# Kernel tuning notes

Measured on AMD Instinct MI355X. Metric: run time of the kernel, lower is better.

The kernel has to match this reference:

```python
import jax, jax.numpy as jnp
import numpy as np

GROUPS = 32
HEADS = 8
EPS = 1e-5


def setup_inputs() -> dict:
    key = jax.random.key(0)
    ks = jax.random.split(key, 3)
    b, c, h, w = 8, 512, 32, 32
    x = jax.random.normal(ks[0], (b, c, h, w), dtype=jnp.float32)
    gn_w = jnp.ones((c,), jnp.float32)
    gn_b = jnp.zeros((c,), jnp.float32)
    qkv_w = jax.random.normal(ks[1], (3 * c, c), dtype=jnp.float32) * (1.0 / np.sqrt(c))
    qkv_b = jnp.zeros((3 * c,), jnp.float32)
    proj_w = jax.random.normal(ks[2], (c, c), dtype=jnp.float32) * (1.0 / np.sqrt(c))
    proj_b = jnp.zeros((c,), jnp.float32)
    return {"x": x, "gn_w": gn_w, "gn_b": gn_b, "qkv_w": qkv_w,
            "qkv_b": qkv_b, "proj_w": proj_w, "proj_b": proj_b}


def group_norm(x, weight, bias):
    b, c, h, w = x.shape
    xg = x.reshape(b, GROUPS, c // GROUPS, h, w)
    mean = xg.mean(axis=(2, 3, 4), keepdims=True)
    var = xg.var(axis=(2, 3, 4), keepdims=True)
    xn = ((xg - mean) * jax.lax.rsqrt(var + EPS)).reshape(b, c, h, w)
    return xn * weight[None, :, None, None] + bias[None, :, None, None]


def reference(x, gn_w, gn_b, qkv_w, qkv_b, proj_w, proj_b):
    b, c, h, w = x.shape
    dh = c // HEADS
    xn = group_norm(x, gn_w, gn_b)
    # 1x1 conv == per-pixel linear: (b,c,h,w) x (3c,c) -> (b,3c,h,w)
    qkv = jnp.einsum('bchw,oc->bohw', xn, qkv_w) + qkv_b[None, :, None, None]
    qkv = qkv.reshape(b, 3, HEADS, dh, h * w)  # 'three' outermost, then heads, head_dim
    q, k, v = qkv[:, 0], qkv[:, 1], qkv[:, 2]  # (b, heads, dh, hw)
    scale = dh ** (-0.5)
    attn = jax.nn.softmax(jnp.einsum('bhci,bhcj->bhij', q, k) * scale, axis=-1)
    out = jnp.einsum('bhij,bhcj->bhci', attn, v)  # (b, heads, dh, hw)
    out = out.reshape(b, c, h, w)
    out = jnp.einsum('bchw,oc->bohw', out, proj_w) + proj_b[None, :, None, None]
    return x + out
```

## Files before the change

### kernel.cpp

```cpp
#include <hip/hip_runtime.h>
#include <cstdint>
#include <cstddef>

#define BATCH 8
#define CCH   512
#define SSP   1024
#define NH    8
#define DH    64
#define O3    1536

typedef __bf16 bf16x8 __attribute__((ext_vector_type(8)));
typedef float  f32x4  __attribute__((ext_vector_type(4)));

__device__ __forceinline__ unsigned short f2bf(float f) {
    unsigned u = __builtin_bit_cast(unsigned, f);
    unsigned r = u + 0x7fffu + ((u >> 16) & 1u);
    return (unsigned short)(r >> 16);
}

__device__ __forceinline__ unsigned pk2bf(float lo, float hi) {
    unsigned ul = __builtin_bit_cast(unsigned, lo) + 0x8000u;
    unsigned uh = __builtin_bit_cast(unsigned, hi) + 0x8000u;
    return __builtin_amdgcn_perm(uh, ul, 0x07060302u);
}

__device__ __forceinline__ bf16x8 ld8(const unsigned short* p) {
    uint4 u = *(const uint4*)p;
    return __builtin_bit_cast(bf16x8, u);
}

__device__ __forceinline__ void glls16(const void* g, void* l) {
    __builtin_amdgcn_global_load_lds(
        (const __attribute__((address_space(1))) unsigned*)g,
        (__attribute__((address_space(3))) unsigned*)l, 16, 0, 0);
}

__global__ __launch_bounds__(256) void wconv2(const float* __restrict__ s1,
                                              unsigned short* __restrict__ d1, int n1,
                                              const float* __restrict__ s2,
                                              unsigned short* __restrict__ d2) {
    int i = blockIdx.x * 256 + threadIdx.x;
    const float4* sp;
    ushort4* dp;
    if (i < n1) { sp = (const float4*)s1 + i; dp = (ushort4*)d1 + i; }
    else        { sp = (const float4*)s2 + (i - n1); dp = (ushort4*)d2 + (i - n1); }
    float4 v = *sp;
    ushort4 o;
    o.x = f2bf(v.x); o.y = f2bf(v.y); o.z = f2bf(v.z); o.w = f2bf(v.w);
    *dp = o;
}

__global__ __launch_bounds__(256) void groupnorm_t(const float* __restrict__ x,
                                                   const float* __restrict__ gw,
                                                   const float* __restrict__ gb,
                                                   unsigned short* __restrict__ xnt) {
    int blk = blockIdx.x;
    int b = blk >> 5, g = blk & 31;
    const float4* xp = (const float4*)(x + (size_t)(b * CCH + g * 16) * SSP);
    int t = threadIdx.x;

    float4 vals[16];
    float sum = 0.f, ss = 0.f;
#pragma unroll
    for (int i = 0; i < 16; i++) {
        float4 v = xp[i * 256 + t];
        vals[i] = v;
        sum += (v.x + v.y) + (v.z + v.w);
        ss  += (v.x * v.x + v.y * v.y) + (v.z * v.z + v.w * v.w);
    }
#pragma unroll
    for (int o = 32; o; o >>= 1) {
        sum += __shfl_xor(sum, o, 64);
        ss  += __shfl_xor(ss,  o, 64);
    }
    __shared__ float red[8];
    if ((t & 63) == 0) { red[(t >> 6) * 2] = sum; red[(t >> 6) * 2 + 1] = ss; }
    __syncthreads();
    sum = red[0] + red[2] + red[4] + red[6];
    ss  = red[1] + red[3] + red[5] + red[7];

    float mean = sum * (1.f / 16384.f);
    float var  = ss * (1.f / 16384.f) - mean * mean;
    float rstd = rsqrtf(var + 1e-5f);

    __shared__ unsigned short tile[16][1032];
#pragma unroll
    for (int i = 0; i < 16; i++) {
        int f4 = i * 256 + t;
        int c = f4 >> 8;
        int s = (f4 & 255) * 4;
        float wsc = gw[g * 16 + c] * rstd;
        float bia = gb[g * 16 + c] - mean * wsc;
        float4 v = vals[i];
        tile[c][s + 0] = f2bf(v.x * wsc + bia);
        tile[c][s + 1] = f2bf(v.y * wsc + bia);
        tile[c][s + 2] = f2bf(v.z * wsc + bia);
        tile[c][s + 3] = f2bf(v.w * wsc + bia);
    }
    __syncthreads();

    int c2 = (t & 7) * 2, sr = t >> 3;
    unsigned short* outbase = xnt + (size_t)b * SSP * CCH + g * 16 + c2;
#pragma unroll
    for (int i = 0; i < 32; i++) {
        int s = i * 32 + sr;
        unsigned v = (unsigned)tile[c2][s] | ((unsigned)tile[c2 + 1][s] << 16);
        *(unsigned*)(outbase + (size_t)s * CCH) = v;
    }
}

__global__ __launch_bounds__(256) void gemm_qkv(const unsigned short* __restrict__ Aall,
                                                const unsigned short* __restrict__ Bw,
                                                const float* __restrict__ bias,
                                                unsigned short* __restrict__ Call,
                                                unsigned short* __restrict__ vtout) {
    const int K = 512;
    int bz = blockIdx.z;
    const unsigned short* A = Aall + (size_t)bz * SSP * CCH;
    int m0 = blockIdx.x * 128, n0 = blockIdx.y * 128;

    __shared__ unsigned short As[128 * 64], Bs[128 * 64];
    int t = threadIdx.x, wave = t >> 6, lane = t & 63;
    int quad = lane >> 4, l16 = lane & 15;
    int wm = (wave & 1) * 64, wn = (wave >> 1) * 64;

    int lrow = lane >> 3;
    int lc   = ((lane & 7) - lrow) & 7;
    const unsigned short* Ag = A  + (size_t)(m0 + wave * 32 + lrow) * K + lc * 8;
    const unsigned short* Bg = Bw + (size_t)(n0 + wave * 32 + lrow) * K + lc * 8;
    unsigned short* Asw = As + wave * 2048;
    unsigned short* Bsw = Bs + wave * 2048;

    f32x4 acc[4][4];
#pragma unroll
    for (int i = 0; i < 4; i++)
#pragma unroll
        for (int j = 0; j < 4; j++) acc[i][j] = f32x4{0.f, 0.f, 0.f, 0.f};

    int rowA = (wm + l16) * 64, rowB = (wn + l16) * 64;
    int cph[2];
#pragma unroll
    for (int kc = 0; kc < 2; kc++) cph[kc] = ((quad + 4 * kc + l16) & 7) * 8;

    for (int k0 = 0; k0 < K; k0 += 64) {
        __syncthreads();
#pragma unroll
        for (int i = 0; i < 4; i++) {
            glls16(Ag + (size_t)i * 8 * K + k0, Asw + i * 512);
            glls16(Bg + (size_t)i * 8 * K + k0, Bsw + i * 512);
        }
        __syncthreads();
#pragma unroll
        for (int kc = 0; kc < 2; kc++) {
            bf16x8 af[4], bfr[4];
#pragma unroll
            for (int i = 0; i < 4; i++) {
                af[i]  = ld8(As + rowA + i * 1024 + cph[kc]);
                bfr[i] = ld8(Bs + rowB + i * 1024 + cph[kc]);
            }
#pragma unroll
            for (int i = 0; i < 4; i++)
#pragma unroll
                for (int j = 0; j < 4; j++)
                    acc[i][j] = __builtin_amdgcn_mfma_f32_16x16x32_bf16(af[i], bfr[j], acc[i][j], 0, 0, 0);
        }
    }

    if (n0 < 1024) {
        unsigned short* Cp = Call + (size_t)bz * SSP * O3;
#pragma unroll
        for (int i = 0; i < 4; i++)
#pragma unroll
            for (int j = 0; j < 4; j++) {
                int col = n0 + wn + j * 16 + l16;
                float bv = bias[col];
#pragma unroll
                for (int r = 0; r < 4; r++) {
                    int row = m0 + wm + i * 16 + quad * 4 + r;
                    Cp[(size_t)row * O3 + col] = f2bf(acc[i][j][r] + bv);
                }
            }
    } else {
#pragma unroll
        for (int j = 0; j < 4; j++) {
            int col = n0 + wn + j * 16 + l16;
            float bv = bias[col];
            unsigned short* vp = vtout + ((size_t)bz * 512 + (col - 1024)) * SSP;
#pragma unroll
            for (int i = 0; i < 4; i++) {
                int s = m0 + wm + i * 16 + quad * 4;
                uint2 d;
                d.x = pk2bf(acc[i][j][0] + bv, acc[i][j][1] + bv);
                d.y = pk2bf(acc[i][j][2] + bv, acc[i][j][3] + bv);
                *(uint2*)(vp + s) = d;
            }
        }
    }
}

__global__ __launch_bounds__(256) void gemm_proj(const unsigned short* __restrict__ Pw,
                                                 const unsigned short* __restrict__ Oall,
                                                 const float* __restrict__ bias,
                                                 const float* __restrict__ xres,
                                                 float* __restrict__ Out) {
    const int K = 512;
    int bz = blockIdx.z;
    const unsigned short* Bv = Oall + (size_t)bz * SSP * CCH;
    int m0 = blockIdx.x * 128, n0 = blockIdx.y * 128;

    __shared__ unsigned short As[128 * 64], Bs[128 * 64];
    int t = threadIdx.x, wave = t >> 6, lane = t & 63;
    int quad = lane >> 4, l16 = lane & 15;
    int wm = (wave & 1) * 64, wn = (wave >> 1) * 64;

    int lrow = lane >> 3;
    int lc   = ((lane & 7) - lrow) & 7;
    const unsigned short* Ag = Pw + (size_t)(m0 + wave * 32 + lrow) * K + lc * 8;
    const unsigned short* Bg = Bv + (size_t)(n0 + wave * 32 + lrow) * K + lc * 8;
    unsigned short* Asw = As + wave * 2048;
    unsigned short* Bsw = Bs + wave * 2048;

    f32x4 acc[4][4];
#pragma unroll
    for (int i = 0; i < 4; i++)
#pragma unroll
        for (int j = 0; j < 4; j++) acc[i][j] = f32x4{0.f, 0.f, 0.f, 0.f};

    int rowA = (wm + l16) * 64, rowB = (wn + l16) * 64;
    int cph[2];
#pragma unroll
    for (int kc = 0; kc < 2; kc++) cph[kc] = ((quad + 4 * kc + l16) & 7) * 8;

    for (int k0 = 0; k0 < K; k0 += 64) {
        __syncthreads();
#pragma unroll
        for (int i = 0; i < 4; i++) {
            glls16(Ag + (size_t)i * 8 * K + k0, Asw + i * 512);
            glls16(Bg + (size_t)i * 8 * K + k0, Bsw + i * 512);
        }
        __syncthreads();
#pragma unroll
        for (int kc = 0; kc < 2; kc++) {
            bf16x8 af[4], bfr[4];
#pragma unroll
            for (int i = 0; i < 4; i++) {
                af[i]  = ld8(As + rowA + i * 1024 + cph[kc]);
                bfr[i] = ld8(Bs + rowB + i * 1024 + cph[kc]);
            }
#pragma unroll
            for (int i = 0; i < 4; i++)
#pragma unroll
                for (int j = 0; j < 4; j++)
                    acc[i][j] = __builtin_amdgcn_mfma_f32_16x16x32_bf16(af[i], bfr[j], acc[i][j], 0, 0, 0);
        }
    }
#pragma unroll
    for (int i = 0; i < 4; i++)
#pragma unroll
        for (int j = 0; j < 4; j++) {
            int col = n0 + wn + j * 16 + l16;
#pragma unroll
            for (int r = 0; r < 4; r++) {
                int row = m0 + wm + i * 16 + quad * 4 + r;
                size_t idx = (size_t)bz * CCH * SSP + (size_t)row * SSP + col;
                Out[idx] = xres[idx] + acc[i][j][r] + bias[row];
            }
        }
}

__global__ __launch_bounds__(256, 4) void attn(const unsigned short* __restrict__ qkvt,
                                               const unsigned short* __restrict__ vt,
                                               unsigned short* __restrict__ ot) {
    int i0 = blockIdx.x * 64;
    int bh = blockIdx.y;
    int b = bh >> 3, h = bh & 7;

    __shared__ unsigned short Ks[128][72];
    __shared__ unsigned short Vs[64][136];

    int t = threadIdx.x, wave = t >> 6, lane = t & 63;
    int quad = lane >> 4, l16 = lane & 15;
    const float c1 = 0.125f * 1.44269504f;

    unsigned short* Ps = &Ks[0][0] + wave * (16 * 136);

    bf16x8 qf[2];
    {
        const unsigned short* qp =
            qkvt + ((size_t)b * SSP + i0 + wave * 16 + l16) * O3 + h * DH + quad * 8;
        qf[0] = ld8(qp);
        qf[1] = ld8(qp + 32);
    }

    f32x4 Oa[4];
#pragma unroll
    for (int i = 0; i < 4; i++) Oa[i] = f32x4{0.f, 0.f, 0.f, 0.f};
    float m_run = -INFINITY, l_run = 0.f;

    int jr = t >> 3, c8 = (t & 7) * 8;
    int cr = t >> 4, j8 = (t & 15) * 8;

    for (int jb = 0; jb < 8; jb++) {
        int j0 = jb * 128;
        __syncthreads();
#pragma unroll
        for (int p = 0; p < 4; p++) {
            int row = p * 32 + jr;
            *(uint4*)&Ks[row][c8] =
                *(const uint4*)(qkvt + ((size_t)b * SSP + j0 + row) * O3 + CCH + h * DH + c8);
        }
#pragma unroll
        for (int p = 0; p < 4; p++) {
            *(uint4*)&Vs[p * 16 + cr][j8] =
                *(const uint4*)(vt + ((size_t)bh * DH + p * 16 + cr) * SSP + j0 + j8);
        }
        __syncthreads();

        f32x4 sc[8];
#pragma unroll
        for (int tj = 0; tj < 8; tj++) sc[tj] = f32x4{0.f, 0.f, 0.f, 0.f};
#pragma unroll
        for (int kc = 0; kc < 2; kc++)
#pragma unroll
            for (int tj = 0; tj < 8; tj++) {
                bf16x8 kf = ld8(&Ks[tj * 16 + l16][kc * 32 + quad * 8]);
                sc[tj] = __builtin_amdgcn_mfma_f32_16x16x32_bf16(kf, qf[kc], sc[tj], 0, 0, 0);
            }

        float m = sc[0][0];
#pragma unroll
        for (int tj = 0; tj < 8; tj++)
#pragma unroll
            for (int r = 0; r < 4; r++) m = fmaxf(m, sc[tj][r]);
        m = fmaxf(m, __shfl_xor(m, 16, 64));
        m = fmaxf(m, __shfl_xor(m, 32, 64));
        float mn = fmaxf(m_run, m);
        float alpha = __builtin_amdgcn_exp2f(c1 * (m_run - mn));
        m_run = mn;
        float cm = c1 * mn;
        float rs = 0.f;
#pragma unroll
        for (int tj = 0; tj < 8; tj++)
#pragma unroll
            for (int r = 0; r < 4; r++) {
                float p = __builtin_amdgcn_exp2f(c1 * sc[tj][r] - cm);
                sc[tj][r] = p;
                rs += p;
            }
        rs += __shfl_xor(rs, 16, 64);
        rs += __shfl_xor(rs, 32, 64);
        l_run = l_run * alpha + rs;

        __syncthreads();

#pragma unroll
        for (int tj = 0; tj < 8; tj++) {
            uint2 d;
            d.x = pk2bf(sc[tj][0], sc[tj][1]);
            d.y = pk2bf(sc[tj][2], sc[tj][3]);
            *(uint2*)&Ps[l16 * 136 + tj * 16 + quad * 4] = d;
        }

#pragma unroll
        for (int tc = 0; tc < 4; tc++)
#pragma unroll
            for (int r = 0; r < 4; r++) Oa[tc][r] *= alpha;
#pragma unroll
        for (int kj = 0; kj < 4; kj++) {
            bf16x8 pf = ld8(&Ps[l16 * 136 + kj * 32 + quad * 8]);
#pragma unroll
            for (int tc = 0; tc < 4; tc++) {
                bf16x8 vf = ld8(&Vs[tc * 16 + l16][kj * 32 + quad * 8]);
                Oa[tc] = __builtin_amdgcn_mfma_f32_16x16x32_bf16(vf, pf, Oa[tc], 0, 0, 0);
            }
        }
    }

    float rl = 1.f / l_run;
    int i = i0 + wave * 16 + l16;
    unsigned short* ob = ot + ((size_t)b * SSP + i) * CCH + h * DH;
#pragma unroll
    for (int tc = 0; tc < 4; tc++) {
        uint2 d;
        d.x = pk2bf(Oa[tc][0] * rl, Oa[tc][1] * rl);
        d.y = pk2bf(Oa[tc][2] * rl, Oa[tc][3] * rl);
        *(uint2*)(ob + tc * 16 + quad * 4) = d;
    }
}

extern "C" void kernel_launch(void* const* d_in, const int* in_sizes, int n_in,
                              void* d_out, int out_size, void* d_ws, size_t ws_size,
                              hipStream_t stream) {
    const float* x      = (const float*)d_in[0];
    const float* gn_w   = (const float*)d_in[1];
    const float* gn_b   = (const float*)d_in[2];
    const float* qkv_w  = (const float*)d_in[3];
    const float* qkv_b  = (const float*)d_in[4];
    const float* proj_w = (const float*)d_in[5];
    const float* proj_b = (const float*)d_in[6];
    float* out = (float*)d_out;

    char* ws = (char*)d_ws;
    unsigned short* xnt   = (unsigned short*)(ws);
    unsigned short* qw_bf = (unsigned short*)(ws + 8388608);
    unsigned short* pw_bf = (unsigned short*)(ws + 9961472);
    unsigned short* qkvt  = (unsigned short*)(ws + 10485760);
    unsigned short* vt    = (unsigned short*)(ws + 35651584);
    unsigned short* otb   = (unsigned short*)(ws + 44040192);

    wconv2<<<dim3(1024), dim3(256), 0, stream>>>(qkv_w, qw_bf, 196608, proj_w, pw_bf);
    groupnorm_t<<<dim3(256), dim3(256), 0, stream>>>(x, gn_w, gn_b, xnt);
    gemm_qkv<<<dim3(8, 12, 8), dim3(256), 0, stream>>>(xnt, qw_bf, qkv_b, qkvt, vt);
    attn<<<dim3(16, 64), dim3(256), 0, stream>>>(qkvt, vt, otb);
    gemm_proj<<<dim3(4, 8, 8), dim3(256), 0, stream>>>(pw_bf, otb, proj_b, x, out);
}
```

Baseline: 163.3 us.

## Fuse weight conversion into groupnorm, shrink proj tile, remap attention blocks per XCD

Merges the weight-to-bf16 conversion and groupnorm into one launch by giving extra blocks the conversion work, which removes one kernel launch. Halves the M tile of the projection GEMM from 128 to 64 so the grid doubles to 512 blocks for better CU fill, at the cost of less operand reuse per block. Remaps the attention grid to a 1D index so blocks of the same batch-head land on the same XCD, aiming for better L2 reuse of K/V.

```diff
diff --git a/kernel.cpp b/kernel.cpp
--- a/kernel.cpp
+++ b/kernel.cpp
@@ -35,29 +35,31 @@
         (__attribute__((address_space(3))) unsigned*)l, 16, 0, 0);
 }
 
-__global__ __launch_bounds__(256) void wconv2(const float* __restrict__ s1,
-                                              unsigned short* __restrict__ d1, int n1,
-                                              const float* __restrict__ s2,
-                                              unsigned short* __restrict__ d2) {
-    int i = blockIdx.x * 256 + threadIdx.x;
-    const float4* sp;
-    ushort4* dp;
-    if (i < n1) { sp = (const float4*)s1 + i; dp = (ushort4*)d1 + i; }
-    else        { sp = (const float4*)s2 + (i - n1); dp = (ushort4*)d2 + (i - n1); }
-    float4 v = *sp;
-    ushort4 o;
-    o.x = f2bf(v.x); o.y = f2bf(v.y); o.z = f2bf(v.z); o.w = f2bf(v.w);
-    *dp = o;
-}
-
-__global__ __launch_bounds__(256) void groupnorm_t(const float* __restrict__ x,
-                                                   const float* __restrict__ gw,
-                                                   const float* __restrict__ gb,
-                                                   unsigned short* __restrict__ xnt) {
+__global__ __launch_bounds__(256) void gn_wconv(const float* __restrict__ x,
+                                                const float* __restrict__ gw,
+                                                const float* __restrict__ gb,
+                                                unsigned short* __restrict__ xnt,
+                                                const float* __restrict__ s1,
+                                                unsigned short* __restrict__ d1, int n1,
+                                                const float* __restrict__ s2,
+                                                unsigned short* __restrict__ d2) {
+    int t = threadIdx.x;
+    if (blockIdx.x >= 256) {
+        int i = (blockIdx.x - 256) * 256 + t;
+        const float4* sp;
+        ushort4* dp;
+        if (i < n1) { sp = (const float4*)s1 + i; dp = (ushort4*)d1 + i; }
+        else        { sp = (const float4*)s2 + (i - n1); dp = (ushort4*)d2 + (i - n1); }
+        float4 v = *sp;
+        ushort4 o;
+        o.x = f2bf(v.x); o.y = f2bf(v.y); o.z = f2bf(v.z); o.w = f2bf(v.w);
+        *dp = o;
+        return;
+    }
+
     int blk = blockIdx.x;
     int b = blk >> 5, g = blk & 31;
     const float4* xp = (const float4*)(x + (size_t)(b * CCH + g * 16) * SSP);
-    int t = threadIdx.x;
 
     float4 vals[16];
     float sum = 0.f, ss = 0.f;
@@ -206,27 +208,27 @@
     const int K = 512;
     int bz = blockIdx.z;
     const unsigned short* Bv = Oall + (size_t)bz * SSP * CCH;
-    int m0 = blockIdx.x * 128, n0 = blockIdx.y * 128;
-
-    __shared__ unsigned short As[128 * 64], Bs[128 * 64];
+    int m0 = blockIdx.x * 64, n0 = blockIdx.y * 128;
+
+    __shared__ unsigned short As[64 * 64], Bs[128 * 64];
     int t = threadIdx.x, wave = t >> 6, lane = t & 63;
     int quad = lane >> 4, l16 = lane & 15;
-    int wm = (wave & 1) * 64, wn = (wave >> 1) * 64;
+    int wr = (wave & 1) * 32, wc = (wave >> 1) * 64;
 
     int lrow = lane >> 3;
     int lc   = ((lane & 7) - lrow) & 7;
-    const unsigned short* Ag = Pw + (size_t)(m0 + wave * 32 + lrow) * K + lc * 8;
+    const unsigned short* Ag = Pw + (size_t)(m0 + wave * 16 + lrow) * K + lc * 8;
     const unsigned short* Bg = Bv + (size_t)(n0 + wave * 32 + lrow) * K + lc * 8;
-    unsigned short* Asw = As + wave * 2048;
+    unsigned short* Asw = As + wave * 1024;
     unsigned short* Bsw = Bs + wave * 2048;
 
-    f32x4 acc[4][4];
-#pragma unroll
-    for (int i = 0; i < 4; i++)
+    f32x4 acc[2][4];
+#pragma unroll
+    for (int i = 0; i < 2; i++)
 #pragma unroll
         for (int j = 0; j < 4; j++) acc[i][j] = f32x4{0.f, 0.f, 0.f, 0.f};
 
-    int rowA = (wm + l16) * 64, rowB = (wn + l16) * 64;
+    int rowA = (wr + l16) * 64, rowB = (wc + l16) * 64;
     int cph[2];
 #pragma unroll
     for (int kc = 0; kc < 2; kc++) cph[kc] = ((quad + 4 * kc + l16) & 7) * 8;
@@ -234,34 +236,34 @@
     for (int k0 = 0; k0 < K; k0 += 64) {
         __syncthreads();
 #pragma unroll
-        for (int i = 0; i < 4; i++) {
+        for (int i = 0; i < 2; i++)
             glls16(Ag + (size_t)i * 8 * K + k0, Asw + i * 512);
+#pragma unroll
+        for (int i = 0; i < 4; i++)
             glls16(Bg + (size_t)i * 8 * K + k0, Bsw + i * 512);
-        }
         __syncthreads();
 #pragma unroll
         for (int kc = 0; kc < 2; kc++) {
-            bf16x8 af[4], bfr[4];
-#pragma unroll
-            for (int i = 0; i < 4; i++) {
-                af[i]  = ld8(As + rowA + i * 1024 + cph[kc]);
-                bfr[i] = ld8(Bs + rowB + i * 1024 + cph[kc]);
-            }
-#pragma unroll
-            for (int i = 0; i < 4; i++)
+            bf16x8 af[2], bfr[4];
+#pragma unroll
+            for (int i = 0; i < 2; i++) af[i]  = ld8(As + rowA + i * 1024 + cph[kc]);
+#pragma unroll
+            for (int j = 0; j < 4; j++) bfr[j] = ld8(Bs + rowB + j * 1024 + cph[kc]);
+#pragma unroll
+            for (int i = 0; i < 2; i++)
 #pragma unroll
                 for (int j = 0; j < 4; j++)
                     acc[i][j] = __builtin_amdgcn_mfma_f32_16x16x32_bf16(af[i], bfr[j], acc[i][j], 0, 0, 0);
         }
     }
 #pragma unroll
-    for (int i = 0; i < 4; i++)
+    for (int i = 0; i < 2; i++)
 #pragma unroll
         for (int j = 0; j < 4; j++) {
-            int col = n0 + wn + j * 16 + l16;
+            int col = n0 + wc + j * 16 + l16;
 #pragma unroll
             for (int r = 0; r < 4; r++) {
-                int row = m0 + wm + i * 16 + quad * 4 + r;
+                int row = m0 + wr + i * 16 + quad * 4 + r;
                 size_t idx = (size_t)bz * CCH * SSP + (size_t)row * SSP + col;
                 Out[idx] = xres[idx] + acc[i][j][r] + bias[row];
             }
@@ -271,8 +273,10 @@
 __global__ __launch_bounds__(256, 4) void attn(const unsigned short* __restrict__ qkvt,
                                                const unsigned short* __restrict__ vt,
                                                unsigned short* __restrict__ ot) {
-    int i0 = blockIdx.x * 64;
-    int bh = blockIdx.y;
+    int blk = blockIdx.x;
+    int xcd = blk & 7, jj = blk >> 3;
+    int bh = xcd * 8 + (jj >> 4);
+    int i0 = (jj & 15) * 64;
     int b = bh >> 3, h = bh & 7;
 
     __shared__ unsigned short Ks[128][72];
@@ -408,9 +412,9 @@
     unsigned short* vt    = (unsigned short*)(ws + 35651584);
     unsigned short* otb   = (unsigned short*)(ws + 44040192);
 
-    wconv2<<<dim3(1024), dim3(256), 0, stream>>>(qkv_w, qw_bf, 196608, proj_w, pw_bf);
-    groupnorm_t<<<dim3(256), dim3(256), 0, stream>>>(x, gn_w, gn_b, xnt);
+    gn_wconv<<<dim3(1280), dim3(256), 0, stream>>>(x, gn_w, gn_b, xnt,
+                                                   qkv_w, qw_bf, 196608, proj_w, pw_bf);
     gemm_qkv<<<dim3(8, 12, 8), dim3(256), 0, stream>>>(xnt, qw_bf, qkv_b, qkvt, vt);
-    attn<<<dim3(16, 64), dim3(256), 0, stream>>>(qkvt, vt, otb);
-    gemm_proj<<<dim3(4, 8, 8), dim3(256), 0, stream>>>(pw_bf, otb, proj_b, x, out);
-}
+    attn<<<dim3(1024), dim3(256), 0, stream>>>(qkvt, vt, otb);
+    gemm_proj<<<dim3(8, 8, 8), dim3(256), 0, stream>>>(pw_bf, otb, proj_b, x, out);
+}
```

After: 163.2 us. Within noise of the previous version (-0.0%).
